# Optimization experiments

Hardware: AMD Instinct MI355X
Metric: run time of the kernel (lower is better)

## Reference

```python
import jax, jax.numpy as jnp
from jax import lax
import numpy as np

C = 256
RATE = 4
NUM_HEADS = 4
WS = 8
EPS = 1e-5


def setup_inputs() -> dict:
    key = jax.random.key(0)
    ks = jax.random.split(key, 24)
    cr = C // RATE  # 64
    s = 0.02
    return {
        "x": jax.random.normal(ks[0], (32, C, 64, 64), jnp.float32),
        # qkv / out projections (stored as [in, out] for x @ W)
        "qkv_w": jax.random.normal(ks[1], (C, 3 * C), jnp.float32) * s,
        "qkv_b": jnp.zeros((3 * C,), jnp.float32),
        "out_w": jax.random.normal(ks[2], (C, C), jnp.float32) * s,
        "out_b": jnp.zeros((C,), jnp.float32),
        # channel-attention MLP
        "ca_w1": jax.random.normal(ks[3], (C, cr), jnp.float32) * s,
        "ca_b1": jnp.zeros((cr,), jnp.float32),
        "ca_w2": jax.random.normal(ks[4], (cr, C), jnp.float32) * s,
        "ca_b2": jnp.zeros((C,), jnp.float32),
        # spatial attention: Conv2d(C, cr, 7, pad=3, groups=cr) -> OIHW (cr, C//cr, 7, 7)
        "sa_w1": jax.random.normal(ks[5], (cr, C // cr, 7, 7), jnp.float32) * s,
        "sa_b1": jnp.zeros((cr,), jnp.float32),
        "bn1_g": jnp.ones((cr,), jnp.float32),
        "bn1_b": jnp.zeros((cr,), jnp.float32),
        "bn1_m": jnp.zeros((cr,), jnp.float32),
        "bn1_v": jnp.ones((cr,), jnp.float32),
        # Conv2d(cr, C, 7, pad=3, groups=cr) -> OIHW (C, 1, 7, 7)
        "sa_w2": jax.random.normal(ks[6], (C, 1, 7, 7), jnp.float32) * s,
        "sa_b2": jnp.zeros((C,), jnp.float32),
        "bn2_g": jnp.ones((C,), jnp.float32),
        "bn2_b": jnp.zeros((C,), jnp.float32),
        "bn2_m": jnp.zeros((C,), jnp.float32),
        "bn2_v": jnp.ones((C,), jnp.float32),
    }


def _bn(y, g, b, m, v):
    # inference-mode BatchNorm2d over channel axis 1
    inv = g / jnp.sqrt(v + EPS)
    return y * inv[None, :, None, None] + (b - m * inv)[None, :, None, None]


def reference(x, qkv_w, qkv_b, out_w, out_b, ca_w1, ca_b1, ca_w2, ca_b2,
              sa_w1, sa_b1, bn1_g, bn1_b, bn1_m, bn1_v,
              sa_w2, sa_b2, bn2_g, bn2_b, bn2_m, bn2_v):
    b, c, h, w = x.shape
    hd = c // NUM_HEADS
    # ---- channel attention gating ----
    xp = x.transpose(0, 2, 3, 1)                      # b,h,w,c
    a = jax.nn.relu(xp @ ca_w1 + ca_b1) @ ca_w2 + ca_b2
    x = x * jax.nn.sigmoid(a.transpose(0, 3, 1, 2))   # b,c,h,w
    # ---- windowed multi-head self-attention ----
    nwh, nww = h // WS, w // WS
    xw = x.reshape(b, c, nwh, WS, nww, WS).transpose(0, 2, 4, 3, 5, 1)
    xw = xw.reshape(-1, WS * WS, c)                   # (b*nwin, 64, c)
    qkv = xw @ qkv_w + qkv_b
    q, k, v = jnp.split(qkv, 3, axis=-1)
    def heads(t):
        return t.reshape(-1, WS * WS, NUM_HEADS, hd).transpose(0, 2, 1, 3)
    q, k, v = heads(q), heads(k), heads(v)            # (nw, H, 64, hd)
    attn = jax.nn.softmax(jnp.einsum('whqd,whkd->whqk', q, k) * (hd ** -0.5), axis=-1)
    o = jnp.einsum('whqk,whkd->whqd', attn, v).transpose(0, 2, 1, 3).reshape(-1, WS * WS, c)
    o = o @ out_w + out_b
    o = o.reshape(b, nwh, nww, WS, WS, c).transpose(0, 5, 1, 3, 2, 4).reshape(b, c, h, w)
    x = x + o
    # ---- channel shuffle (groups=4) ----
    g = 4
    x = x.reshape(b, g, c // g, h, w).transpose(0, 2, 1, 3, 4).reshape(b, c, h, w)
    # ---- spatial attention branch ----
    dn = ('NCHW', 'OIHW', 'NCHW')
    cr = c // RATE
    y = lax.conv_general_dilated(x, sa_w1, (1, 1), [(3, 3), (3, 3)],
                                 dimension_numbers=dn, feature_group_count=cr)
    y = _bn(y + sa_b1[None, :, None, None], bn1_g, bn1_b, bn1_m, bn1_v)
    y = jax.nn.relu(y)
    y = lax.conv_general_dilated(y, sa_w2, (1, 1), [(3, 3), (3, 3)],
                                 dimension_numbers=dn, feature_group_count=cr)
    y = _bn(y + sa_b2[None, :, None, None], bn2_g, bn2_b, bn2_m, bn2_v)
    return x * jax.nn.sigmoid(y)
```

## Files before the change

### kernel.cpp

```cpp
#include <hip/hip_runtime.h>

#define HW 4096
#define CCH 256

typedef __bf16 bf16x8 __attribute__((ext_vector_type(8)));
typedef float f32x4 __attribute__((ext_vector_type(4)));
typedef float f32x2 __attribute__((ext_vector_type(2)));
typedef unsigned u32x2 __attribute__((ext_vector_type(2)));
typedef unsigned short u16;

#define SWZ8(r) ((((r) + ((r) >> 2)) & 7) << 3)

__device__ __forceinline__ u16 f2b(float f) {
  union { __bf16 h; u16 u; } c; c.h = (__bf16)f; return c.u;
}
__device__ __forceinline__ unsigned f2b2(float a, float b) {
  union { __bf16 h[2]; unsigned u; } c;
  c.h[0] = (__bf16)a; c.h[1] = (__bf16)b; return c.u;
}
__device__ __forceinline__ float b2f(u16 h) {
  union { unsigned u; float f; } v; v.u = ((unsigned)h) << 16; return v.f;
}
__device__ __forceinline__ void nt_store4(const float4& v, float* p) {
  f32x4 t; t[0] = v.x; t[1] = v.y; t[2] = v.z; t[3] = v.w;
  __builtin_nontemporal_store(t, reinterpret_cast<f32x4*>(p));
}

__global__ __launch_bounds__(256) void kprep(
    const float* __restrict__ qkv_w, const float* __restrict__ out_w,
    const float* __restrict__ ca_w1, const float* __restrict__ ca_w2,
    u16* __restrict__ wq2, u16* __restrict__ wo2,
    u16* __restrict__ c1f, u16* __restrict__ c2f)
{
  int i = blockIdx.x * 256 + threadIdx.x;
  int j = i & 7, lane = (i >> 3) & 63, l15 = lane & 15, lg = lane >> 4;
  if (i < 48 * 8 * 512) {
    int kb = (i >> 9) & 7, T = i >> 12;
    wq2[i] = f2b(qkv_w[(kb * 32 + lg * 8 + j) * 768 + T * 16 + l15]);
  }
  if (i < 16 * 8 * 512) {
    int kb = (i >> 9) & 7, T = i >> 12;
    wo2[i] = f2b(out_w[(kb * 32 + lg * 8 + j) * 256 + T * 16 + l15]);
  }
  if (i < 4 * 8 * 512) {
    int kb = (i >> 9) & 7, T = i >> 12;
    c1f[i] = f2b(ca_w1[(kb * 32 + lg * 8 + j) * 64 + T * 16 + l15]);
  }
  if (i < 16 * 2 * 512) {
    int kb = (i >> 9) & 1, T = i >> 10;
    c2f[i] = f2b(ca_w2[(kb * 32 + lg * 8 + j) * 256 + T * 16 + l15]);
  }
}

__global__ __launch_bounds__(256, 4) void kb_attn(
    const float* __restrict__ x, u16* __restrict__ x2w, u16* __restrict__ Og,
    const u16* __restrict__ wq2, const float* __restrict__ qkv_b,
    const float* __restrict__ out_b,
    const u16* __restrict__ c1f, const float* __restrict__ ca_b1,
    const u16* __restrict__ c2f, const float* __restrict__ ca_b2)
{
  __shared__ u16 smem[20480];
  u16* pX  = smem;
  u16* pH  = smem + 16384;
  u16* pQ  = smem;
  u16* pK  = smem + 4096;
  u16* pVT = smem + 8192;

  const int tid = threadIdx.x;
  const int lane = tid & 63;
  const int wv = __builtin_amdgcn_readfirstlane(tid >> 6);
  const int l15 = lane & 15;
  const int lg = lane >> 4;

  const int bid = blockIdx.x;
  const int wid = (bid & 7) * 256 + (bid >> 3);
  const int b = wid >> 6, wrem = wid & 63;
  const int pbase = (wrem >> 3) * (8 * 64) + (wrem & 7) * 8;
  const float* ximg = x + (size_t)b * CCH * HW;

  const int tokA = wv * 16 + l15;
  const int swA = SWZ8(tokA);

  {
    const int t0 = l15 * 4;
    const int prow = pbase + (l15 >> 1) * 64 + (l15 & 1) * 4;
    #pragma unroll 2
    for (int i = 0; i < 16; ++i) {
      int c = i * 16 + wv * 4 + lg;
      const float4 v = *reinterpret_cast<const float4*>(&ximg[(size_t)c * HW + prow]);
      pX[(t0 + 0) * 256 + (c ^ SWZ8(t0 + 0))] = f2b(v.x);
      pX[(t0 + 1) * 256 + (c ^ SWZ8(t0 + 1))] = f2b(v.y);
      pX[(t0 + 2) * 256 + (c ^ SWZ8(t0 + 2))] = f2b(v.z);
      pX[(t0 + 3) * 256 + (c ^ SWZ8(t0 + 3))] = f2b(v.w);
    }
  }
  __syncthreads();

  uint2 gpk[16];
  {
    bf16x8 aXr[8];
    #pragma unroll
    for (int kb = 0; kb < 8; ++kb)
      aXr[kb] = *reinterpret_cast<const bf16x8*>(&pX[tokA * 256 + ((kb * 32 + lg * 8) ^ swA)]);
    #pragma unroll
    for (int nt1 = 0; nt1 < 4; ++nt1) {
      f32x4 c1 = {0.f, 0.f, 0.f, 0.f};
      #pragma unroll
      for (int kb = 0; kb < 8; ++kb) {
        bf16x8 bw = *reinterpret_cast<const bf16x8*>(&c1f[(nt1 * 8 + kb) * 512 + lane * 8]);
        c1 = __builtin_amdgcn_mfma_f32_16x16x32_bf16(bw, aXr[kb], c1, 0, 0, 0);
      }
      const float4 b14 = *reinterpret_cast<const float4*>(&ca_b1[nt1 * 16 + lg * 4]);
      uint2 pk;
      pk.x = f2b2(fmaxf(c1[0] + b14.x, 0.f), fmaxf(c1[1] + b14.y, 0.f));
      pk.y = f2b2(fmaxf(c1[2] + b14.z, 0.f), fmaxf(c1[3] + b14.w, 0.f));
      int d0 = nt1 * 16 + lg * 4;
      *reinterpret_cast<uint2*>(&pH[tokA * 64 + (d0 ^ swA)]) = pk;
    }
    bf16x8 hB[2];
    #pragma unroll
    for (int kb = 0; kb < 2; ++kb)
      hB[kb] = *reinterpret_cast<const bf16x8*>(&pH[tokA * 64 + ((kb * 32 + lg * 8) ^ swA)]);
    #pragma unroll
    for (int nt = 0; nt < 16; ++nt) {
      f32x4 a2 = {0.f, 0.f, 0.f, 0.f};
      #pragma unroll
      for (int kb = 0; kb < 2; ++kb) {
        bf16x8 w2a = *reinterpret_cast<const bf16x8*>(&c2f[(nt * 2 + kb) * 512 + lane * 8]);
        a2 = __builtin_amdgcn_mfma_f32_16x16x32_bf16(w2a, hB[kb], a2, 0, 0, 0);
      }
      const int n0 = nt * 16 + lg * 4;
      const float4 b24 = *reinterpret_cast<const float4*>(&ca_b2[n0]);
      const ushort4 xq = *reinterpret_cast<const ushort4*>(&pX[tokA * 256 + (n0 ^ swA)]);
      float xg0 = b2f(xq.x) / (1.f + __expf(-(a2[0] + b24.x)));
      float xg1 = b2f(xq.y) / (1.f + __expf(-(a2[1] + b24.y)));
      float xg2 = b2f(xq.z) / (1.f + __expf(-(a2[2] + b24.z)));
      float xg3 = b2f(xq.w) / (1.f + __expf(-(a2[3] + b24.w)));
      uint2 pk;
      pk.x = f2b2(xg0, xg1);
      pk.y = f2b2(xg2, xg3);
      gpk[nt] = pk;
      *reinterpret_cast<uint2*>(&pX[tokA * 256 + (n0 ^ swA)]) = pk;
    }
  }

  {
    u16* wout = x2w + (size_t)wid * 16384;
    #pragma unroll
    for (int nt0 = 0; nt0 < 4; ++nt0) {
      #pragma unroll
      for (int r = 0; r < 4; ++r) {
        int cq = nt0 * 16 + lg * 4 + r;
        unsigned v0 = (r < 2) ? (gpk[nt0     ].x >> (16 * r)) : (gpk[nt0     ].y >> (16 * (r - 2)));
        unsigned v1 = (r < 2) ? (gpk[nt0 +  4].x >> (16 * r)) : (gpk[nt0 +  4].y >> (16 * (r - 2)));
        unsigned v2 = (r < 2) ? (gpk[nt0 +  8].x >> (16 * r)) : (gpk[nt0 +  8].y >> (16 * (r - 2)));
        unsigned v3 = (r < 2) ? (gpk[nt0 + 12].x >> (16 * r)) : (gpk[nt0 + 12].y >> (16 * (r - 2)));
        u32x2 o;
        o[0] = f2b2(b2f((u16)v0) + out_b[cq],       b2f((u16)v1) + out_b[cq + 64]);
        o[1] = f2b2(b2f((u16)v2) + out_b[cq + 128], b2f((u16)v3) + out_b[cq + 192]);
        __builtin_nontemporal_store(o, reinterpret_cast<u32x2*>(&wout[cq * 256 + tokA * 4]));
      }
    }
  }

  bf16x8 aG[8];
  #pragma unroll
  for (int kb = 0; kb < 8; ++kb)
    aG[kb] = *reinterpret_cast<const bf16x8*>(&pX[tokA * 256 + ((kb * 32 + lg * 8) ^ swA)]);
  __syncthreads();

  u16* ogw = Og + (size_t)wid * 16384;

  for (int h = 0; h < 4; ++h) {
    #pragma unroll 2
    for (int tau = 0; tau < 12; ++tau) {
      int kind = tau >> 2, sub = tau & 3;
      int colbase = kind * 256 + h * 64 + sub * 16;
      int T = kind * 16 + h * 4 + sub;
      f32x4 acc = {0.f, 0.f, 0.f, 0.f};
      #pragma unroll
      for (int kb = 0; kb < 8; ++kb) {
        bf16x8 bw = *reinterpret_cast<const bf16x8*>(&wq2[(T * 8 + kb) * 512 + lane * 8]);
        acc = __builtin_amdgcn_mfma_f32_16x16x32_bf16(bw, aG[kb], acc, 0, 0, 0);
      }
      const float4 bia4 = *reinterpret_cast<const float4*>(&qkv_b[colbase + lg * 4]);
      if (kind == 2) {
        #pragma unroll
        for (int r = 0; r < 4; ++r) {
          int d = sub * 16 + lg * 4 + r;
          float bv = (r == 0) ? bia4.x : (r == 1) ? bia4.y : (r == 2) ? bia4.z : bia4.w;
          pVT[d * 64 + (tokA ^ ((d & 7) << 3))] = f2b(acc[r] + bv);
        }
      } else {
        uint2 pk;
        pk.x = f2b2(acc[0] + bia4.x, acc[1] + bia4.y);
        pk.y = f2b2(acc[2] + bia4.z, acc[3] + bia4.w);
        int d0 = sub * 16 + lg * 4;
        u16* dst = (kind == 0) ? pQ : pK;
        *reinterpret_cast<uint2*>(&dst[tokA * 64 + (d0 ^ swA)]) = pk;
      }
    }
    __syncthreads();

    bf16x8 aQ[2];
    #pragma unroll
    for (int kb = 0; kb < 2; ++kb)
      aQ[kb] = *reinterpret_cast<const bf16x8*>(&pQ[tokA * 64 + ((kb * 32 + lg * 8) ^ swA)]);
    f32x4 s4[4];
    #pragma unroll
    for (int jt = 0; jt < 4; ++jt) {
      int krow = jt * 16 + l15;
      int swk = SWZ8(krow);
      f32x4 acc = {0.f, 0.f, 0.f, 0.f};
      #pragma unroll
      for (int kb = 0; kb < 2; ++kb) {
        bf16x8 bK = *reinterpret_cast<const bf16x8*>(&pK[krow * 64 + ((kb * 32 + lg * 8) ^ swk)]);
        acc = __builtin_amdgcn_mfma_f32_16x16x32_bf16(aQ[kb], bK, acc, 0, 0, 0);
      }
      s4[jt] = acc;
    }
    #pragma unroll
    for (int r = 0; r < 4; ++r) {
      float m = fmaxf(fmaxf(s4[0][r], s4[1][r]), fmaxf(s4[2][r], s4[3][r]));
      #pragma unroll
      for (int off = 1; off < 16; off <<= 1) m = fmaxf(m, __shfl_xor(m, off));
      float e0 = __expf((s4[0][r] - m) * 0.125f);
      float e1 = __expf((s4[1][r] - m) * 0.125f);
      float e2 = __expf((s4[2][r] - m) * 0.125f);
      float e3 = __expf((s4[3][r] - m) * 0.125f);
      float sum = e0 + e1 + e2 + e3;
      #pragma unroll
      for (int off = 1; off < 16; off <<= 1) sum += __shfl_xor(sum, off);
      float is = 1.f / sum;
      int tok = wv * 16 + lg * 4 + r;
      int swp = SWZ8(tok);
      pQ[tok * 64 + ((     l15) ^ swp)] = f2b(e0 * is);
      pQ[tok * 64 + ((16 + l15) ^ swp)] = f2b(e1 * is);
      pQ[tok * 64 + ((32 + l15) ^ swp)] = f2b(e2 * is);
      pQ[tok * 64 + ((48 + l15) ^ swp)] = f2b(e3 * is);
    }
    bf16x8 bP[2];
    #pragma unroll
    for (int kb = 0; kb < 2; ++kb)
      bP[kb] = *reinterpret_cast<const bf16x8*>(&pQ[tokA * 64 + ((kb * 32 + lg * 8) ^ swA)]);
    #pragma unroll
    for (int dt = 0; dt < 4; ++dt) {
      int drow = dt * 16 + l15;
      int swd = (drow & 7) << 3;
      f32x4 acc = {0.f, 0.f, 0.f, 0.f};
      #pragma unroll
      for (int kb = 0; kb < 2; ++kb) {
        bf16x8 aV = *reinterpret_cast<const bf16x8*>(&pVT[drow * 64 + ((kb * 32 + lg * 8) ^ swd)]);
        acc = __builtin_amdgcn_mfma_f32_16x16x32_bf16(aV, bP[kb], acc, 0, 0, 0);
      }
      int d0 = h * 64 + dt * 16 + lg * 4;
      uint2 pk;
      pk.x = f2b2(acc[0], acc[1]);
      pk.y = f2b2(acc[2], acc[3]);
      *reinterpret_cast<uint2*>(&ogw[(d0 >> 2) * 256 + tokA * 4]) = pk;
    }
    __syncthreads();
  }
}

__global__ __launch_bounds__(256, 3) void kb_oproj(
    const u16* __restrict__ Og, const u16* __restrict__ wo2,
    u16* __restrict__ x2w)
{
  const int tid = threadIdx.x;
  const int lane = tid & 63;
  const int wv = __builtin_amdgcn_readfirstlane(tid >> 6);
  const int l15 = lane & 15;
  const int lg = lane >> 4;
  const int bid = blockIdx.x;
  const int wid = (bid & 7) * 256 + (bid >> 3);
  const int tokA = wv * 16 + l15;

  const u16* og = Og + (size_t)wid * 16384;
  bf16x8 bO[8];
  #pragma unroll
  for (int kb = 0; kb < 8; ++kb) {
    int dq = kb * 8 + lg * 2;
    uint2 lo = *reinterpret_cast<const uint2*>(&og[dq * 256 + tokA * 4]);
    uint2 hi = *reinterpret_cast<const uint2*>(&og[(dq + 1) * 256 + tokA * 4]);
    union { uint4 u; bf16x8 v; } cvt;
    cvt.u.x = lo.x; cvt.u.y = lo.y; cvt.u.z = hi.x; cvt.u.w = hi.y;
    bO[kb] = cvt.v;
  }

  f32x4 acc[16];
  #pragma unroll
  for (int nt = 0; nt < 16; ++nt) {
    f32x4 z = {0.f, 0.f, 0.f, 0.f};
    acc[nt] = z;
  }
  #pragma unroll
  for (int nt = 0; nt < 16; ++nt) {
    #pragma unroll
    for (int kb = 0; kb < 8; ++kb) {
      bf16x8 wA = *reinterpret_cast<const bf16x8*>(&wo2[(nt * 8 + kb) * 512 + lane * 8]);
      acc[nt] = __builtin_amdgcn_mfma_f32_16x16x32_bf16(wA, bO[kb], acc[nt], 0, 0, 0);
    }
  }

  u16* wout = x2w + (size_t)wid * 16384;
  #pragma unroll
  for (int nt0 = 0; nt0 < 4; ++nt0) {
    #pragma unroll
    for (int r = 0; r < 4; ++r) {
      int cq = nt0 * 16 + lg * 4 + r;
      u16* p = &wout[cq * 256 + tokA * 4];
      uint2 cur = *reinterpret_cast<const uint2*>(p);
      float c0 = b2f((u16)(cur.x & 0xffff)) + acc[nt0     ][r];
      float c1 = b2f((u16)(cur.x >> 16))    + acc[nt0 +  4][r];
      float c2 = b2f((u16)(cur.y & 0xffff)) + acc[nt0 +  8][r];
      float c3 = b2f((u16)(cur.y >> 16))    + acc[nt0 + 12][r];
      uint2 o;
      o.x = f2b2(c0, c1);
      o.y = f2b2(c2, c3);
      *reinterpret_cast<uint2*>(p) = o;
    }
  }
}

__global__ __launch_bounds__(256) void kc_conv1(
    const u16* __restrict__ x2w, const float* __restrict__ w1, const float* __restrict__ b1,
    const float* __restrict__ g1, const float* __restrict__ bb1,
    const float* __restrict__ m1, const float* __restrict__ v1,
    u16* __restrict__ y1)
{
  __shared__ float sin_[4 * 22 * 72];
  const int bid = blockIdx.x;
  const int wid = (bid & 7) * 1024 + (bid >> 3);
  int b = wid >> 8, rem = wid & 255, j = rem >> 2, qt = rem & 3;
  const u16* xw = x2w + (size_t)b * 64 * 16384;
  for (int idx = threadIdx.x; idx < 22 * 70; idx += 256) {
    int yy = idx / 70, xx = idx - yy * 70;
    int ih = qt * 16 + yy - 3, iw = xx - 3;
    uint2 v = {0u, 0u};
    if (ih >= 0 && ih < 64 && iw >= 0 && iw < 64) {
      int wr = (ih >> 3) * 8 + (iw >> 3);
      int tok = (ih & 7) * 8 + (iw & 7);
      v = *reinterpret_cast<const uint2*>(&xw[(size_t)wr * 16384 + j * 256 + tok * 4]);
    }
    sin_[0 * 1584 + yy * 72 + xx] = b2f((u16)(v.x & 0xffff));
    sin_[1 * 1584 + yy * 72 + xx] = b2f((u16)(v.x >> 16));
    sin_[2 * 1584 + yy * 72 + xx] = b2f((u16)(v.y & 0xffff));
    sin_[3 * 1584 + yy * 72 + xx] = b2f((u16)(v.y >> 16));
  }
  __syncthreads();

  float inv = g1[j] / sqrtf(v1[j] + 1e-5f);
  float shf = bb1[j] - m1[j] * inv;
  float bia = b1[j];
  u16* yo = y1 + ((size_t)b * 64 + j) * HW + qt * 16 * 64;
  const float* wbase = w1 + j * 4 * 49;

  int y = threadIdx.x >> 4, x4 = (threadIdx.x & 15) * 4;
  float a0 = 0.f, a1 = 0.f, a2 = 0.f, a3 = 0.f;
  for (int i = 0; i < 4; ++i) {
    #pragma unroll
    for (int ky = 0; ky < 7; ++ky) {
      const float* row = sin_ + (i * 22 + y + ky) * 72 + x4;
      const f32x4 p0 = *reinterpret_cast<const f32x4*>(row);
      const f32x4 p1 = *reinterpret_cast<const f32x4*>(row + 4);
      const f32x2 p2 = *reinterpret_cast<const f32x2*>(row + 8);
      float v[10] = {p0[0], p0[1], p0[2], p0[3], p1[0], p1[1], p1[2], p1[3], p2[0], p2[1]};
      const float* wr = wbase + (i * 7 + ky) * 7;
      #pragma unroll
      for (int kx = 0; kx < 7; ++kx) {
        float wvv = wr[kx];
        a0 += v[kx] * wvv; a1 += v[kx+1] * wvv;
        a2 += v[kx+2] * wvv; a3 += v[kx+3] * wvv;
      }
    }
  }
  u32x2 o;
  o[0] = f2b2(fmaxf((a0 + bia) * inv + shf, 0.f), fmaxf((a1 + bia) * inv + shf, 0.f));
  o[1] = f2b2(fmaxf((a2 + bia) * inv + shf, 0.f), fmaxf((a3 + bia) * inv + shf, 0.f));
  __builtin_nontemporal_store(o, reinterpret_cast<u32x2*>(yo + y * 64 + x4));
}

__global__ __launch_bounds__(256) void kd_conv2(
    const u16* __restrict__ y1, const u16* __restrict__ x2w,
    const float* __restrict__ w2, const float* __restrict__ b2,
    const float* __restrict__ g2, const float* __restrict__ bb2,
    const float* __restrict__ m2, const float* __restrict__ v2,
    float* __restrict__ out)
{
  __shared__ float sin_[70 * 72];
  const int bid = blockIdx.x;
  const int wid = (bid & 7) * 256 + (bid >> 3);
  int b = wid >> 6, g = wid & 63;
  const u16* yin = y1 + ((size_t)b * 64 + g) * HW;

  for (int idx = threadIdx.x; idx < 6 * 72; idx += 256) {
    int r = idx / 72, c = idx - r * 72;
    sin_[(r < 3 ? r : 64 + r) * 72 + c] = 0.f;
  }
  for (int idx = threadIdx.x; idx < 64 * 6; idx += 256) {
    int r = idx / 6, c = idx - r * 6;
    sin_[(r + 3) * 72 + (c < 3 ? c : 64 + c)] = 0.f;
  }
  for (int idx = threadIdx.x; idx < 64 * 16; idx += 256) {
    int r = idx >> 4, c4 = (idx & 15) * 4;
    uint2 v = *reinterpret_cast<const uint2*>(&yin[r * 64 + c4]);
    float* d = &sin_[(r + 3) * 72 + 3 + c4];
    d[0] = b2f((u16)(v.x & 0xffff)); d[1] = b2f((u16)(v.x >> 16));
    d[2] = b2f((u16)(v.y & 0xffff)); d[3] = b2f((u16)(v.y >> 16));
  }
  __syncthreads();

  float inv[4], shf[4], bia[4];
  #pragma unroll
  for (int i = 0; i < 4; ++i) {
    int n = 4 * g + i;
    float sc = g2[n] / sqrtf(v2[n] + 1e-5f);
    inv[i] = sc; shf[i] = bb2[n] - m2[n] * sc; bia[i] = b2[n];
  }
  const float* wb = w2 + 4 * g * 49;
  const u16* xw = x2w + (size_t)b * 64 * 16384;

  for (int it = 0; it < 4; ++it) {
    int s = it * 256 + threadIdx.x;
    int y = s >> 4, x4 = (s & 15) * 4;
    float acc[4][4] = {};
    #pragma unroll
    for (int ky = 0; ky < 7; ++ky) {
      const float* row = sin_ + (y + ky) * 72 + x4;
      const f32x4 p0 = *reinterpret_cast<const f32x4*>(row);
      const f32x4 p1 = *reinterpret_cast<const f32x4*>(row + 4);
      const f32x2 p2 = *reinterpret_cast<const f32x2*>(row + 8);
      float v[10] = {p0[0], p0[1], p0[2], p0[3], p1[0], p1[1], p1[2], p1[3], p2[0], p2[1]};
      #pragma unroll
      for (int i = 0; i < 4; ++i) {
        const float* wr = wb + i * 49 + ky * 7;
        #pragma unroll
        for (int kx = 0; kx < 7; ++kx) {
          float wvv = wr[kx];
          acc[i][0] += v[kx] * wvv; acc[i][1] += v[kx+1] * wvv;
          acc[i][2] += v[kx+2] * wvv; acc[i][3] += v[kx+3] * wvv;
        }
      }
    }
    int po = y * 64 + x4;
    int wr_ = (y >> 3) * 8 + (x4 >> 3);
    int t0 = (y & 7) * 8 + (x4 & 7);
    const u16* gp = &xw[(size_t)wr_ * 16384 + g * 256 + t0 * 4];
    uint2 q0 = *reinterpret_cast<const uint2*>(gp + 0);
    uint2 q1 = *reinterpret_cast<const uint2*>(gp + 4);
    uint2 q2 = *reinterpret_cast<const uint2*>(gp + 8);
    uint2 q3 = *reinterpret_cast<const uint2*>(gp + 12);
    #pragma unroll
    for (int i = 0; i < 4; ++i) {
      int n = 4 * g + i;
      float* op = out + ((size_t)b * 256 + n) * HW + po;
      float y0 = (acc[i][0] + bia[i]) * inv[i] + shf[i];
      float y1v = (acc[i][1] + bia[i]) * inv[i] + shf[i];
      float y2 = (acc[i][2] + bia[i]) * inv[i] + shf[i];
      float y3 = (acc[i][3] + bia[i]) * inv[i] + shf[i];
      float g0 = b2f((u16)(i < 2 ? (q0.x >> (16 * i)) : (q0.y >> (16 * (i - 2)))));
      float g1v = b2f((u16)(i < 2 ? (q1.x >> (16 * i)) : (q1.y >> (16 * (i - 2)))));
      float g2v = b2f((u16)(i < 2 ? (q2.x >> (16 * i)) : (q2.y >> (16 * (i - 2)))));
      float g3 = b2f((u16)(i < 2 ? (q3.x >> (16 * i)) : (q3.y >> (16 * (i - 2)))));
      float4 r;
      r.x = g0  / (1.f + __expf(-y0));
      r.y = g1v / (1.f + __expf(-y1v));
      r.z = g2v / (1.f + __expf(-y2));
      r.w = g3  / (1.f + __expf(-y3));
      nt_store4(r, op);
    }
  }
}

extern "C" void kernel_launch(void* const* d_in, const int* in_sizes, int n_in,
                              void* d_out, int out_size, void* d_ws, size_t ws_size,
                              hipStream_t stream) {
  const float* x     = (const float*)d_in[0];
  const float* qkv_w = (const float*)d_in[1];
  const float* qkv_b = (const float*)d_in[2];
  const float* out_w = (const float*)d_in[3];
  const float* out_b = (const float*)d_in[4];
  const float* ca_w1 = (const float*)d_in[5];
  const float* ca_b1 = (const float*)d_in[6];
  const float* ca_w2 = (const float*)d_in[7];
  const float* ca_b2 = (const float*)d_in[8];
  const float* sa_w1 = (const float*)d_in[9];
  const float* sa_b1 = (const float*)d_in[10];
  const float* bn1_g = (const float*)d_in[11];
  const float* bn1_b = (const float*)d_in[12];
  const float* bn1_m = (const float*)d_in[13];
  const float* bn1_v = (const float*)d_in[14];
  const float* sa_w2 = (const float*)d_in[15];
  const float* sa_b2 = (const float*)d_in[16];
  const float* bn2_g = (const float*)d_in[17];
  const float* bn2_b = (const float*)d_in[18];
  const float* bn2_m = (const float*)d_in[19];
  const float* bn2_v = (const float*)d_in[20];

  float* outp = (float*)d_out;
  u16* x2w = (u16*)d_ws;
  u16* y1 = x2w + (size_t)2048 * 16384;

  u16* wq2 = (u16*)d_out;
  u16* wo2 = wq2 + 48 * 8 * 512;
  u16* c1f = wo2 + 16 * 8 * 512;
  u16* c2f = c1f + 4 * 8 * 512;
  u16* Og  = c2f + 16 * 2 * 512;

  kprep   <<<768,  256, 0, stream>>>(qkv_w, out_w, ca_w1, ca_w2, wq2, wo2, c1f, c2f);
  kb_attn <<<2048, 256, 0, stream>>>(x, x2w, Og, wq2, qkv_b, out_b, c1f, ca_b1, c2f, ca_b2);
  kb_oproj<<<2048, 256, 0, stream>>>(Og, wo2, x2w);
  kc_conv1<<<8192, 256, 0, stream>>>(x2w, sa_w1, sa_b1, bn1_g, bn1_b, bn1_m, bn1_v, y1);
  kd_conv2<<<2048, 256, 0, stream>>>(y1, x2w, sa_w2, sa_b2, bn2_g, bn2_b, bn2_m, bn2_v, outp);
}
```

Measured before the change: 424.2 us.

## Fuse output projection into attention kernel, accumulating per-head in registers

Removes the separate kb_oproj kernel and the Og global buffer. Each head's attention output is staged through shared memory and multiplied by its slice of the output-projection weights, accumulating into 16 fp32 register tiles seeded with the gated residual plus bias. The combined residual is written once instead of being written, re-read and rewritten. This costs many more registers, so launch bounds drop from 4 to 3 blocks per SM, and the residual is now summed in fp32 rather than rounded to bf16 first.

```diff
diff --git a/kernel.cpp b/kernel.cpp
--- a/kernel.cpp
+++ b/kernel.cpp
@@ -52,10 +52,10 @@
   }
 }
 
-__global__ __launch_bounds__(256, 4) void kb_attn(
-    const float* __restrict__ x, u16* __restrict__ x2w, u16* __restrict__ Og,
+__global__ __launch_bounds__(256, 3) void kb_attn(
+    const float* __restrict__ x, u16* __restrict__ x2w,
     const u16* __restrict__ wq2, const float* __restrict__ qkv_b,
-    const float* __restrict__ out_b,
+    const u16* __restrict__ wo2, const float* __restrict__ out_b,
     const u16* __restrict__ c1f, const float* __restrict__ ca_b1,
     const u16* __restrict__ c2f, const float* __restrict__ ca_b2)
 {
@@ -96,7 +96,7 @@
   }
   __syncthreads();
 
-  uint2 gpk[16];
+  f32x4 acc_out[16];
   {
     bf16x8 aXr[8];
     #pragma unroll
@@ -131,35 +131,20 @@
       }
       const int n0 = nt * 16 + lg * 4;
       const float4 b24 = *reinterpret_cast<const float4*>(&ca_b2[n0]);
+      const float4 ob4 = *reinterpret_cast<const float4*>(&out_b[n0]);
       const ushort4 xq = *reinterpret_cast<const ushort4*>(&pX[tokA * 256 + (n0 ^ swA)]);
       float xg0 = b2f(xq.x) / (1.f + __expf(-(a2[0] + b24.x)));
       float xg1 = b2f(xq.y) / (1.f + __expf(-(a2[1] + b24.y)));
       float xg2 = b2f(xq.z) / (1.f + __expf(-(a2[2] + b24.z)));
       float xg3 = b2f(xq.w) / (1.f + __expf(-(a2[3] + b24.w)));
+      acc_out[nt][0] = xg0 + ob4.x;
+      acc_out[nt][1] = xg1 + ob4.y;
+      acc_out[nt][2] = xg2 + ob4.z;
+      acc_out[nt][3] = xg3 + ob4.w;
       uint2 pk;
       pk.x = f2b2(xg0, xg1);
       pk.y = f2b2(xg2, xg3);
-      gpk[nt] = pk;
       *reinterpret_cast<uint2*>(&pX[tokA * 256 + (n0 ^ swA)]) = pk;
-    }
-  }
-
-  {
-    u16* wout = x2w + (size_t)wid * 16384;
-    #pragma unroll
-    for (int nt0 = 0; nt0 < 4; ++nt0) {
-      #pragma unroll
-      for (int r = 0; r < 4; ++r) {
-        int cq = nt0 * 16 + lg * 4 + r;
-        unsigned v0 = (r < 2) ? (gpk[nt0     ].x >> (16 * r)) : (gpk[nt0     ].y >> (16 * (r - 2)));
-        unsigned v1 = (r < 2) ? (gpk[nt0 +  4].x >> (16 * r)) : (gpk[nt0 +  4].y >> (16 * (r - 2)));
-        unsigned v2 = (r < 2) ? (gpk[nt0 +  8].x >> (16 * r)) : (gpk[nt0 +  8].y >> (16 * (r - 2)));
-        unsigned v3 = (r < 2) ? (gpk[nt0 + 12].x >> (16 * r)) : (gpk[nt0 + 12].y >> (16 * (r - 2)));
-        u32x2 o;
-        o[0] = f2b2(b2f((u16)v0) + out_b[cq],       b2f((u16)v1) + out_b[cq + 64]);
-        o[1] = f2b2(b2f((u16)v2) + out_b[cq + 128], b2f((u16)v3) + out_b[cq + 192]);
-        __builtin_nontemporal_store(o, reinterpret_cast<u32x2*>(&wout[cq * 256 + tokA * 4]));
-      }
     }
   }
 
@@ -168,8 +153,6 @@
   for (int kb = 0; kb < 8; ++kb)
     aG[kb] = *reinterpret_cast<const bf16x8*>(&pX[tokA * 256 + ((kb * 32 + lg * 8) ^ swA)]);
   __syncthreads();
-
-  u16* ogw = Og + (size_t)wid * 16384;
 
   for (int h = 0; h < 4; ++h) {
     #pragma unroll 2
@@ -243,6 +226,7 @@
     #pragma unroll
     for (int kb = 0; kb < 2; ++kb)
       bP[kb] = *reinterpret_cast<const bf16x8*>(&pQ[tokA * 64 + ((kb * 32 + lg * 8) ^ swA)]);
+    f32x4 o4[4];
     #pragma unroll
     for (int dt = 0; dt < 4; ++dt) {
       int drow = dt * 16 + l15;
@@ -253,72 +237,43 @@
         bf16x8 aV = *reinterpret_cast<const bf16x8*>(&pVT[drow * 64 + ((kb * 32 + lg * 8) ^ swd)]);
         acc = __builtin_amdgcn_mfma_f32_16x16x32_bf16(aV, bP[kb], acc, 0, 0, 0);
       }
-      int d0 = h * 64 + dt * 16 + lg * 4;
+      o4[dt] = acc;
+    }
+    #pragma unroll
+    for (int dt = 0; dt < 4; ++dt) {
+      int d0 = dt * 16 + lg * 4;
       uint2 pk;
-      pk.x = f2b2(acc[0], acc[1]);
-      pk.y = f2b2(acc[2], acc[3]);
-      *reinterpret_cast<uint2*>(&ogw[(d0 >> 2) * 256 + tokA * 4]) = pk;
+      pk.x = f2b2(o4[dt][0], o4[dt][1]);
+      pk.y = f2b2(o4[dt][2], o4[dt][3]);
+      *reinterpret_cast<uint2*>(&pQ[tokA * 64 + (d0 ^ swA)]) = pk;
+    }
+    bf16x8 bO[2];
+    #pragma unroll
+    for (int kb = 0; kb < 2; ++kb)
+      bO[kb] = *reinterpret_cast<const bf16x8*>(&pQ[tokA * 64 + ((kb * 32 + lg * 8) ^ swA)]);
+    #pragma unroll
+    for (int nt = 0; nt < 16; ++nt) {
+      #pragma unroll
+      for (int kb = 0; kb < 2; ++kb) {
+        bf16x8 wA = *reinterpret_cast<const bf16x8*>(&wo2[(nt * 8 + h * 2 + kb) * 512 + lane * 8]);
+        acc_out[nt] = __builtin_amdgcn_mfma_f32_16x16x32_bf16(wA, bO[kb], acc_out[nt], 0, 0, 0);
+      }
     }
     __syncthreads();
   }
-}
-
-__global__ __launch_bounds__(256, 3) void kb_oproj(
-    const u16* __restrict__ Og, const u16* __restrict__ wo2,
-    u16* __restrict__ x2w)
-{
-  const int tid = threadIdx.x;
-  const int lane = tid & 63;
-  const int wv = __builtin_amdgcn_readfirstlane(tid >> 6);
-  const int l15 = lane & 15;
-  const int lg = lane >> 4;
-  const int bid = blockIdx.x;
-  const int wid = (bid & 7) * 256 + (bid >> 3);
-  const int tokA = wv * 16 + l15;
-
-  const u16* og = Og + (size_t)wid * 16384;
-  bf16x8 bO[8];
-  #pragma unroll
-  for (int kb = 0; kb < 8; ++kb) {
-    int dq = kb * 8 + lg * 2;
-    uint2 lo = *reinterpret_cast<const uint2*>(&og[dq * 256 + tokA * 4]);
-    uint2 hi = *reinterpret_cast<const uint2*>(&og[(dq + 1) * 256 + tokA * 4]);
-    union { uint4 u; bf16x8 v; } cvt;
-    cvt.u.x = lo.x; cvt.u.y = lo.y; cvt.u.z = hi.x; cvt.u.w = hi.y;
-    bO[kb] = cvt.v;
-  }
-
-  f32x4 acc[16];
-  #pragma unroll
-  for (int nt = 0; nt < 16; ++nt) {
-    f32x4 z = {0.f, 0.f, 0.f, 0.f};
-    acc[nt] = z;
-  }
-  #pragma unroll
-  for (int nt = 0; nt < 16; ++nt) {
-    #pragma unroll
-    for (int kb = 0; kb < 8; ++kb) {
-      bf16x8 wA = *reinterpret_cast<const bf16x8*>(&wo2[(nt * 8 + kb) * 512 + lane * 8]);
-      acc[nt] = __builtin_amdgcn_mfma_f32_16x16x32_bf16(wA, bO[kb], acc[nt], 0, 0, 0);
-    }
-  }
-
-  u16* wout = x2w + (size_t)wid * 16384;
-  #pragma unroll
-  for (int nt0 = 0; nt0 < 4; ++nt0) {
-    #pragma unroll
-    for (int r = 0; r < 4; ++r) {
-      int cq = nt0 * 16 + lg * 4 + r;
-      u16* p = &wout[cq * 256 + tokA * 4];
-      uint2 cur = *reinterpret_cast<const uint2*>(p);
-      float c0 = b2f((u16)(cur.x & 0xffff)) + acc[nt0     ][r];
-      float c1 = b2f((u16)(cur.x >> 16))    + acc[nt0 +  4][r];
-      float c2 = b2f((u16)(cur.y & 0xffff)) + acc[nt0 +  8][r];
-      float c3 = b2f((u16)(cur.y >> 16))    + acc[nt0 + 12][r];
-      uint2 o;
-      o.x = f2b2(c0, c1);
-      o.y = f2b2(c2, c3);
-      *reinterpret_cast<uint2*>(p) = o;
+
+  {
+    u16* wout = x2w + (size_t)wid * 16384;
+    #pragma unroll
+    for (int nt0 = 0; nt0 < 4; ++nt0) {
+      #pragma unroll
+      for (int r = 0; r < 4; ++r) {
+        int cq = nt0 * 16 + lg * 4 + r;
+        u32x2 o;
+        o[0] = f2b2(acc_out[nt0     ][r], acc_out[nt0 +  4][r]);
+        o[1] = f2b2(acc_out[nt0 +  8][r], acc_out[nt0 + 12][r]);
+        __builtin_nontemporal_store(o, reinterpret_cast<u32x2*>(&wout[cq * 256 + tokA * 4]));
+      }
     }
   }
 }
@@ -506,11 +461,9 @@
   u16* wo2 = wq2 + 48 * 8 * 512;
   u16* c1f = wo2 + 16 * 8 * 512;
   u16* c2f = c1f + 4 * 8 * 512;
-  u16* Og  = c2f + 16 * 2 * 512;
 
   kprep   <<<768,  256, 0, stream>>>(qkv_w, out_w, ca_w1, ca_w2, wq2, wo2, c1f, c2f);
-  kb_attn <<<2048, 256, 0, stream>>>(x, x2w, Og, wq2, qkv_b, out_b, c1f, ca_b1, c2f, ca_b2);
-  kb_oproj<<<2048, 256, 0, stream>>>(Og, wo2, x2w);
+  kb_attn <<<2048, 256, 0, stream>>>(x, x2w, wq2, qkv_b, wo2, out_b, c1f, ca_b1, c2f, ca_b2);
   kc_conv1<<<8192, 256, 0, stream>>>(x2w, sa_w1, sa_b1, bn1_g, bn1_b, bn1_m, bn1_v, y1);
   kd_conv2<<<2048, 256, 0, stream>>>(y1, x2w, sa_w2, sa_b2, bn2_g, bn2_b, bn2_m, bn2_v, outp);
 }
```

Result: slower. 449.6 us (+6.0%).

## Split gating and attention into separate kernels to reduce LDS and raise occupancy

Applied to the files above, without the earlier changes.

The fused gate+attention kernel is split in two. The first computes the channel-attention gating, writes x2w, and stores the gated bf16 tokens in MFMA-fragment order to a new workspace buffer. The second kernel loads those fragments directly, uses a smaller shared-memory footprint (24KB instead of 40KB), and requests 6 blocks per CU instead of 4. This adds an extra global round trip of about 32MB of bf16 plus a kernel launch, in exchange for higher occupancy in the attention stage.

```diff
diff --git a/kernel.cpp b/kernel.cpp
--- a/kernel.cpp
+++ b/kernel.cpp
@@ -7,6 +7,7 @@
 typedef float f32x4 __attribute__((ext_vector_type(4)));
 typedef float f32x2 __attribute__((ext_vector_type(2)));
 typedef unsigned u32x2 __attribute__((ext_vector_type(2)));
+typedef unsigned u32x4 __attribute__((ext_vector_type(4)));
 typedef unsigned short u16;
 
 #define SWZ8(r) ((((r) + ((r) >> 2)) & 7) << 3)
@@ -52,19 +53,15 @@
   }
 }
 
-__global__ __launch_bounds__(256, 4) void kb_attn(
-    const float* __restrict__ x, u16* __restrict__ x2w, u16* __restrict__ Og,
-    const u16* __restrict__ wq2, const float* __restrict__ qkv_b,
+__global__ __launch_bounds__(256, 4) void kg_gate(
+    const float* __restrict__ x, u16* __restrict__ x2w, u16* __restrict__ xgf,
     const float* __restrict__ out_b,
     const u16* __restrict__ c1f, const float* __restrict__ ca_b1,
     const u16* __restrict__ c2f, const float* __restrict__ ca_b2)
 {
   __shared__ u16 smem[20480];
-  u16* pX  = smem;
-  u16* pH  = smem + 16384;
-  u16* pQ  = smem;
-  u16* pK  = smem + 4096;
-  u16* pVT = smem + 8192;
+  u16* pX = smem;
+  u16* pH = smem + 16384;
 
   const int tid = threadIdx.x;
   const int lane = tid & 63;
@@ -163,11 +160,44 @@
     }
   }
 
+  {
+    u16* xo = xgf + ((size_t)wid * 4 + wv) * 4096;
+    #pragma unroll
+    for (int kb = 0; kb < 8; ++kb) {
+      union { bf16x8 v; u32x4 u; } c;
+      c.v = *reinterpret_cast<const bf16x8*>(&pX[tokA * 256 + ((kb * 32 + lg * 8) ^ swA)]);
+      __builtin_nontemporal_store(c.u, reinterpret_cast<u32x4*>(&xo[kb * 512 + lane * 8]));
+    }
+  }
+}
+
+__global__ __launch_bounds__(256, 6) void ka_attn(
+    const u16* __restrict__ xgf, u16* __restrict__ Og,
+    const u16* __restrict__ wq2, const float* __restrict__ qkv_b)
+{
+  __shared__ u16 smem[12288];
+  u16* pQ  = smem;
+  u16* pK  = smem + 4096;
+  u16* pVT = smem + 8192;
+
+  const int tid = threadIdx.x;
+  const int lane = tid & 63;
+  const int wv = __builtin_amdgcn_readfirstlane(tid >> 6);
+  const int l15 = lane & 15;
+  const int lg = lane >> 4;
+
+  const int bid = blockIdx.x;
+  const int wid = (bid & 7) * 256 + (bid >> 3);
+  const int tokA = wv * 16 + l15;
+  const int swA = SWZ8(tokA);
+
   bf16x8 aG[8];
-  #pragma unroll
-  for (int kb = 0; kb < 8; ++kb)
-    aG[kb] = *reinterpret_cast<const bf16x8*>(&pX[tokA * 256 + ((kb * 32 + lg * 8) ^ swA)]);
-  __syncthreads();
+  {
+    const u16* xi = xgf + ((size_t)wid * 4 + wv) * 4096;
+    #pragma unroll
+    for (int kb = 0; kb < 8; ++kb)
+      aG[kb] = *reinterpret_cast<const bf16x8*>(&xi[kb * 512 + lane * 8]);
+  }
 
   u16* ogw = Og + (size_t)wid * 16384;
 
@@ -501,6 +531,7 @@
   float* outp = (float*)d_out;
   u16* x2w = (u16*)d_ws;
   u16* y1 = x2w + (size_t)2048 * 16384;
+  u16* xgf = y1 + (size_t)8 * 1024 * 1024;
 
   u16* wq2 = (u16*)d_out;
   u16* wo2 = wq2 + 48 * 8 * 512;
@@ -509,7 +540,8 @@
   u16* Og  = c2f + 16 * 2 * 512;
 
   kprep   <<<768,  256, 0, stream>>>(qkv_w, out_w, ca_w1, ca_w2, wq2, wo2, c1f, c2f);
-  kb_attn <<<2048, 256, 0, stream>>>(x, x2w, Og, wq2, qkv_b, out_b, c1f, ca_b1, c2f, ca_b2);
+  kg_gate <<<2048, 256, 0, stream>>>(x, x2w, xgf, out_b, c1f, ca_b1, c2f, ca_b2);
+  ka_attn <<<2048, 256, 0, stream>>>(xgf, Og, wq2, qkv_b);
   kb_oproj<<<2048, 256, 0, stream>>>(Og, wo2, x2w);
   kc_conv1<<<8192, 256, 0, stream>>>(x2w, sa_w1, sa_b1, bn1_g, bn1_b, bn1_m, bn1_v, y1);
   kd_conv2<<<2048, 256, 0, stream>>>(y1, x2w, sa_w2, sa_b2, bn2_g, bn2_b, bn2_m, bn2_v, outp);
```

Result: slower. 594.3 us (+40.1%).
